# Kernel tuning notes

Measured on AMD Instinct MI355X. Metric: run time of the kernel, lower is better.

## Reference

```python
import jax, jax.numpy as jnp
import numpy as np

STRIDE = 2
PAD = 1
K = 4
OUT_PAD = 0


def setup_inputs() -> dict:
    key = jax.random.key(0)
    k1, k2, k3, k4 = jax.random.split(key, 4)
    x = jax.random.normal(k1, (16, 64, 128, 128), dtype=jnp.float32)
    # torch ConvTranspose2d weight layout: [in_channels, out_channels, kH, kW]
    w = jax.random.normal(k2, (64, 32, 4, 4), dtype=jnp.float32) * 0.05
    conv_b = jax.random.normal(k3, (32,), dtype=jnp.float32) * 0.05
    bias = jax.random.normal(k4, (1, 1, 1, 1), dtype=jnp.float32)
    return {"x": x, "w": w, "conv_b": conv_b, "bias": bias}


def conv_transpose2d(x, w, conv_b):
    # Equivalent of torch ConvTranspose2d(k=4, s=2, p=1, op=0):
    # dilate input by stride, pad by k-1-p (+op on trailing side), conv with flipped kernel.
    lo = K - 1 - PAD
    hi = K - 1 - PAD + OUT_PAD
    w_oihw = jnp.flip(w, axis=(2, 3)).transpose(1, 0, 2, 3)  # [Cout, Cin, kH, kW]
    y = jax.lax.conv_general_dilated(
        x, w_oihw,
        window_strides=(1, 1),
        padding=((lo, hi), (lo, hi)),
        lhs_dilation=(STRIDE, STRIDE),
        dimension_numbers=("NCHW", "OIHW", "NCHW"),
    )
    return y + conv_b[None, :, None, None]


def reference(x, w, conv_b, bias):
    y = conv_transpose2d(x, w, conv_b)          # [N, Cout, H', W']
    y = jnp.min(y, axis=1, keepdims=True)       # channel-min -> [N,1,H',W']
    y = jnp.sum(y, axis=2, keepdims=True)       # height-sum  -> [N,1,1,W']
    # kernel uses tanh-based GELU approximation
    return jax.nn.gelu(y, approximate=True) + bias
```

## Files before the change

kernel.cpp:

```cpp
#include <hip/hip_runtime.h>
#include <math.h>

typedef __attribute__((ext_vector_type(8))) short short8;
typedef __attribute__((ext_vector_type(16))) float f32x16;

#define XS_STRIDE 72

__device__ __forceinline__ short f2bf(float f) {
    union { float f; unsigned u; } v; v.f = f;
    unsigned r = (v.u + 0x7FFFu + ((v.u >> 16) & 1u)) >> 16;
    return (short)r;
}

__global__ void zero_acc(float* __restrict__ acc) {
    acc[blockIdx.x * 256 + threadIdx.x] = 0.f;
}

__global__ void build_wfrag(const float* __restrict__ w, short* __restrict__ wfrag) {
    int idx = blockIdx.x * 256 + threadIdx.x;
    int j    = idx & 7;
    int lane = (idx >> 3) & 63;
    int q    = (idx >> 9) & 15;
    int p    = idx >> 13;
    int co = lane & 31, half = lane >> 5;
    int ci = (q & 3) * 16 + half * 8 + j;
    int t = q >> 2, a = t >> 1, b = t & 1;
    int ph = p >> 1, pw = p & 1;
    int kh = 2 * a + 1 - ph, kw = 2 * b + 1 - pw;
    wfrag[idx] = f2bf(w[((ci * 32 + co) * 4 + kh) * 4 + kw]);
}

__global__ __launch_bounds__(256, 4) void convt_mfma(
    const float* __restrict__ x, const short* __restrict__ wfrag,
    const float* __restrict__ conv_b, float* __restrict__ acc4096)
{
    __shared__ short xs[4][66][XS_STRIDE];
    __shared__ float minbuf[2][4][64];

    int blk = blockIdx.x;
    int jh = blk & 1;
    int i0 = ((blk >> 1) & 63) * 2;
    int n  = blk >> 7;
    int t  = threadIdx.x;

    {
        int col  = t & 63;
        int cih  = (t >> 6) * 4;
        int gcol = jh * 64 + col;
        for (int r = 0; r < 4; ++r) {
            int gi = i0 - 1 + r;
            bool rowok = (unsigned)gi < 128u;
            int gic = rowok ? gi : 0;
            for (int g = 0; g < 4; ++g) {
                int ci = g * 16 + cih;
                const float* px = x + (((size_t)(n * 64 + ci) * 128 + gic) * 128 + gcol);
                float v0 = rowok ? px[0]     : 0.f;
                float v1 = rowok ? px[16384] : 0.f;
                float v2 = rowok ? px[32768] : 0.f;
                float v3 = rowok ? px[49152] : 0.f;
                union { short s[4]; unsigned long long u; } pk;
                pk.s[0] = f2bf(v0); pk.s[1] = f2bf(v1);
                pk.s[2] = f2bf(v2); pk.s[3] = f2bf(v3);
                *(unsigned long long*)&xs[r][col + 1][ci] = pk.u;
            }
        }
        {
            int r = t >> 6, ci = t & 63, gi = i0 - 1 + r;
            for (int side = 0; side < 2; ++side) {
                int gc = jh * 64 + (side ? 64 : -1);
                float v = ((unsigned)gi < 128u && (unsigned)gc < 128u)
                        ? x[((size_t)(n * 64 + ci) * 128 + gi) * 128 + gc] : 0.f;
                xs[r][side ? 65 : 0][ci] = f2bf(v);
            }
        }
    }
    __syncthreads();

    int wv = t >> 6, lane = t & 63;
    int ph = wv >> 1, pw = wv & 1;
    int ln = lane & 31, half = lane >> 5;

    short8 af[16];
    const short8* wf = (const short8*)(wfrag + wv * 8192);
    #pragma unroll
    for (int q = 0; q < 16; ++q) af[q] = wf[q * 64 + lane];

    float cb[16];
    #pragma unroll
    for (int reg = 0; reg < 16; ++reg) {
        int co = (reg & 3) + 8 * (reg >> 2) + 4 * half;
        cb[reg] = conv_b[co];
    }

    #pragma unroll
    for (int rp = 0; rp < 2; ++rp) {
        for (int j0 = 0; j0 < 64; j0 += 32) {
            f32x16 acc;
            #pragma unroll
            for (int reg = 0; reg < 16; ++reg) acc[reg] = cb[reg];
            #pragma unroll
            for (int q = 0; q < 16; ++q) {
                int tq = q >> 2, a = tq >> 1, b = tq & 1;
                int ridx = rp + 1 + ph - a;
                int colp = j0 + ln + (pw - b) + 1;
                int ci0  = (q & 3) * 16 + half * 8;
                const short8* bp = (const short8*)&xs[ridx][colp][ci0];
                acc = __builtin_amdgcn_mfma_f32_32x32x16_bf16(af[q], *bp, acc, 0, 0, 0);
            }
            float mn = acc[0];
            #pragma unroll
            for (int reg = 1; reg < 16; ++reg) mn = fminf(mn, acc[reg]);
            mn = fminf(mn, __shfl_xor(mn, 32, 64));
            if (half == 0) minbuf[rp][wv][j0 + ln] = mn;
        }
    }
    __syncthreads();

    {
        int rp  = t >> 7;
        int pw2 = (t >> 6) & 1;
        int jl  = t & 63;
        float v = minbuf[rp][pw2][jl] + minbuf[rp][2 + pw2][jl];
        int ow = ((jh * 64 + jl) << 1) | pw2;
        atomicAdd(&acc4096[n * 256 + ow], v);
    }
}

__global__ void finalize(const float* __restrict__ acc4096,
                         const float* __restrict__ bias, float* __restrict__ out)
{
    int idx = blockIdx.x * 256 + threadIdx.x;
    float s = acc4096[idx];
    float u = 0.7978845608028654f * (s + 0.044715f * s * s * s);
    out[idx] = 0.5f * s * (1.f + tanhf(u)) + bias[0];
}

extern "C" void kernel_launch(void* const* d_in, const int* in_sizes, int n_in,
                              void* d_out, int out_size, void* d_ws, size_t ws_size,
                              hipStream_t stream) {
    const float* x      = (const float*)d_in[0];
    const float* w      = (const float*)d_in[1];
    const float* conv_b = (const float*)d_in[2];
    const float* bias   = (const float*)d_in[3];
    float* out = (float*)d_out;

    float* acc   = (float*)d_ws;
    short* wfrag = (short*)((char*)d_ws + 16384);

    hipLaunchKernelGGL(zero_acc, dim3(16), dim3(256), 0, stream, acc);
    hipLaunchKernelGGL(build_wfrag, dim3(128), dim3(256), 0, stream, w, wfrag);
    hipLaunchKernelGGL(convt_mfma, dim3(16 * 64 * 2), dim3(256), 0, stream,
                       x, wfrag, conv_b, acc);
    hipLaunchKernelGGL(finalize, dim3(16), dim3(256), 0, stream,
                       acc, bias, out);
}
```

Measured before the change: 135.5 us.

## Fuse prep kernels and fold finalize into last-block epilogue

Merges the zero and weight-fragment kernels into a single prep launch and removes the separate finalize launch. The last conv block to finish, detected with a global atomic counter, applies GELU and bias to the accumulated sums. Each block also pre-sums both row pairs before its atomicAdd, halving the atomics. This cuts two launches and the gaps between them, at the cost of a threadfence and counter atomic per block plus a serial epilogue run by one block.

```diff
diff --git a/kernel.cpp b/kernel.cpp
--- a/kernel.cpp
+++ b/kernel.cpp
@@ -5,6 +5,7 @@
 typedef __attribute__((ext_vector_type(16))) float f32x16;
 
 #define XS_STRIDE 72
+#define NBLOCKS (16 * 64 * 2)
 
 __device__ __forceinline__ short f2bf(float f) {
     union { float f; unsigned u; } v; v.f = f;
@@ -12,30 +13,36 @@
     return (short)r;
 }
 
-__global__ void zero_acc(float* __restrict__ acc) {
-    acc[blockIdx.x * 256 + threadIdx.x] = 0.f;
-}
-
-__global__ void build_wfrag(const float* __restrict__ w, short* __restrict__ wfrag) {
-    int idx = blockIdx.x * 256 + threadIdx.x;
-    int j    = idx & 7;
-    int lane = (idx >> 3) & 63;
-    int q    = (idx >> 9) & 15;
-    int p    = idx >> 13;
-    int co = lane & 31, half = lane >> 5;
-    int ci = (q & 3) * 16 + half * 8 + j;
-    int t = q >> 2, a = t >> 1, b = t & 1;
-    int ph = p >> 1, pw = p & 1;
-    int kh = 2 * a + 1 - ph, kw = 2 * b + 1 - pw;
-    wfrag[idx] = f2bf(w[((ci * 32 + co) * 4 + kh) * 4 + kw]);
+__global__ void prep(const float* __restrict__ w, short* __restrict__ wfrag,
+                     float* __restrict__ acc, unsigned* __restrict__ counter) {
+    int b = blockIdx.x, t = threadIdx.x;
+    if (b < 128) {
+        int idx = b * 256 + t;
+        int j    = idx & 7;
+        int lane = (idx >> 3) & 63;
+        int q    = (idx >> 9) & 15;
+        int p    = idx >> 13;
+        int co = lane & 31, half = lane >> 5;
+        int ci = (q & 3) * 16 + half * 8 + j;
+        int tp = q >> 2, a = tp >> 1, bb = tp & 1;
+        int ph = p >> 1, pw = p & 1;
+        int kh = 2 * a + 1 - ph, kw = 2 * bb + 1 - pw;
+        wfrag[idx] = f2bf(w[((ci * 32 + co) * 4 + kh) * 4 + kw]);
+    } else {
+        acc[(b - 128) * 256 + t] = 0.f;
+        if (b == 128 && t == 0) *counter = 0u;
+    }
 }
 
 __global__ __launch_bounds__(256, 4) void convt_mfma(
     const float* __restrict__ x, const short* __restrict__ wfrag,
-    const float* __restrict__ conv_b, float* __restrict__ acc4096)
+    const float* __restrict__ conv_b, const float* __restrict__ bias,
+    float* __restrict__ acc4096, unsigned* __restrict__ counter,
+    float* __restrict__ out)
 {
     __shared__ short xs[4][66][XS_STRIDE];
     __shared__ float minbuf[2][4][64];
+    __shared__ unsigned lastflag;
 
     int blk = blockIdx.x;
     int jh = blk & 1;
@@ -116,23 +123,32 @@
     }
     __syncthreads();
 
-    {
-        int rp  = t >> 7;
+    if (t < 128) {
         int pw2 = (t >> 6) & 1;
         int jl  = t & 63;
-        float v = minbuf[rp][pw2][jl] + minbuf[rp][2 + pw2][jl];
+        float v = minbuf[0][pw2][jl] + minbuf[0][2 + pw2][jl]
+                + minbuf[1][pw2][jl] + minbuf[1][2 + pw2][jl];
         int ow = ((jh * 64 + jl) << 1) | pw2;
         atomicAdd(&acc4096[n * 256 + ow], v);
     }
-}
+    __threadfence();
+    __syncthreads();
 
-__global__ void finalize(const float* __restrict__ acc4096,
-                         const float* __restrict__ bias, float* __restrict__ out)
-{
-    int idx = blockIdx.x * 256 + threadIdx.x;
-    float s = acc4096[idx];
-    float u = 0.7978845608028654f * (s + 0.044715f * s * s * s);
-    out[idx] = 0.5f * s * (1.f + tanhf(u)) + bias[0];
+    if (t == 0) {
+        unsigned old = __hip_atomic_fetch_add(counter, 1u, __ATOMIC_ACQ_REL,
+                                              __HIP_MEMORY_SCOPE_AGENT);
+        lastflag = (old == (unsigned)(NBLOCKS - 1)) ? 1u : 0u;
+    }
+    __syncthreads();
+    if (lastflag) {
+        float b0 = bias[0];
+        for (int k = t; k < 4096; k += 256) {
+            float s = __hip_atomic_load(&acc4096[k], __ATOMIC_RELAXED,
+                                        __HIP_MEMORY_SCOPE_AGENT);
+            float u = 0.7978845608028654f * (s + 0.044715f * s * s * s);
+            out[k] = 0.5f * s * (1.f + tanhf(u)) + b0;
+        }
+    }
 }
 
 extern "C" void kernel_launch(void* const* d_in, const int* in_sizes, int n_in,
@@ -144,13 +160,11 @@
     const float* bias   = (const float*)d_in[3];
     float* out = (float*)d_out;
 
-    float* acc   = (float*)d_ws;
-    short* wfrag = (short*)((char*)d_ws + 16384);
+    float*    acc     = (float*)d_ws;
+    unsigned* counter = (unsigned*)((char*)d_ws + 16384);
+    short*    wfrag   = (short*)((char*)d_ws + 16448);
 
-    hipLaunchKernelGGL(zero_acc, dim3(16), dim3(256), 0, stream, acc);
-    hipLaunchKernelGGL(build_wfrag, dim3(128), dim3(256), 0, stream, w, wfrag);
-    hipLaunchKernelGGL(convt_mfma, dim3(16 * 64 * 2), dim3(256), 0, stream,
-                       x, wfrag, conv_b, acc);
-    hipLaunchKernelGGL(finalize, dim3(16), dim3(256), 0, stream,
-                       acc, bias, out);
+    hipLaunchKernelGGL(prep, dim3(144), dim3(256), 0, stream, w, wfrag, acc, counter);
+    hipLaunchKernelGGL(convt_mfma, dim3(NBLOCKS), dim3(256), 0, stream,
+                       x, wfrag, conv_b, bias, acc, counter, out);
 }
```

Result: slower. 298.8 us (+120.6%).

## Fuse all stages into one persistent cooperative kernel with grid sync

Applied to the files above, without the earlier changes.

Replaces the four launches (zero, weight-fragment build, conv, finalize) with one persistent cooperative kernel. Each block builds its bf16 weight fragments directly from w, loops over work items, and writes deterministic per-row-pair partials instead of atomics. After a grid-wide sync, 16 blocks reduce the partials and apply GELU plus bias. This removes launch overhead and atomic contention, at the cost of redundant weight conversion per block, a grid-sync barrier and a synchronous occupancy query on the host.

```diff
diff --git a/kernel.cpp b/kernel.cpp
--- a/kernel.cpp
+++ b/kernel.cpp
@@ -1,10 +1,14 @@
 #include <hip/hip_runtime.h>
+#include <hip/hip_cooperative_groups.h>
 #include <math.h>
+
+namespace cg = cooperative_groups;
 
 typedef __attribute__((ext_vector_type(8))) short short8;
 typedef __attribute__((ext_vector_type(16))) float f32x16;
 
 #define XS_STRIDE 72
+#define NITEMS (16 * 64 * 2)
 
 __device__ __forceinline__ short f2bf(float f) {
     union { float f; unsigned u; } v; v.f = f;
@@ -12,127 +16,121 @@
     return (short)r;
 }
 
-__global__ void zero_acc(float* __restrict__ acc) {
-    acc[blockIdx.x * 256 + threadIdx.x] = 0.f;
-}
-
-__global__ void build_wfrag(const float* __restrict__ w, short* __restrict__ wfrag) {
-    int idx = blockIdx.x * 256 + threadIdx.x;
-    int j    = idx & 7;
-    int lane = (idx >> 3) & 63;
-    int q    = (idx >> 9) & 15;
-    int p    = idx >> 13;
-    int co = lane & 31, half = lane >> 5;
-    int ci = (q & 3) * 16 + half * 8 + j;
-    int t = q >> 2, a = t >> 1, b = t & 1;
-    int ph = p >> 1, pw = p & 1;
-    int kh = 2 * a + 1 - ph, kw = 2 * b + 1 - pw;
-    wfrag[idx] = f2bf(w[((ci * 32 + co) * 4 + kh) * 4 + kw]);
-}
-
-__global__ __launch_bounds__(256, 4) void convt_mfma(
-    const float* __restrict__ x, const short* __restrict__ wfrag,
-    const float* __restrict__ conv_b, float* __restrict__ acc4096)
+__global__ __launch_bounds__(256, 4) void convt_fused(
+    const float* __restrict__ x, const float* __restrict__ w,
+    const float* __restrict__ conv_b, const float* __restrict__ bias,
+    float* __restrict__ partial, float* __restrict__ out)
 {
     __shared__ short xs[4][66][XS_STRIDE];
     __shared__ float minbuf[2][4][64];
 
-    int blk = blockIdx.x;
-    int jh = blk & 1;
-    int i0 = ((blk >> 1) & 63) * 2;
-    int n  = blk >> 7;
-    int t  = threadIdx.x;
-
-    {
-        int col  = t & 63;
-        int cih  = (t >> 6) * 4;
-        int gcol = jh * 64 + col;
-        for (int r = 0; r < 4; ++r) {
-            int gi = i0 - 1 + r;
-            bool rowok = (unsigned)gi < 128u;
-            int gic = rowok ? gi : 0;
-            for (int g = 0; g < 4; ++g) {
-                int ci = g * 16 + cih;
-                const float* px = x + (((size_t)(n * 64 + ci) * 128 + gic) * 128 + gcol);
-                float v0 = rowok ? px[0]     : 0.f;
-                float v1 = rowok ? px[16384] : 0.f;
-                float v2 = rowok ? px[32768] : 0.f;
-                float v3 = rowok ? px[49152] : 0.f;
-                union { short s[4]; unsigned long long u; } pk;
-                pk.s[0] = f2bf(v0); pk.s[1] = f2bf(v1);
-                pk.s[2] = f2bf(v2); pk.s[3] = f2bf(v3);
-                *(unsigned long long*)&xs[r][col + 1][ci] = pk.u;
-            }
-        }
-        {
-            int r = t >> 6, ci = t & 63, gi = i0 - 1 + r;
-            for (int side = 0; side < 2; ++side) {
-                int gc = jh * 64 + (side ? 64 : -1);
-                float v = ((unsigned)gi < 128u && (unsigned)gc < 128u)
-                        ? x[((size_t)(n * 64 + ci) * 128 + gi) * 128 + gc] : 0.f;
-                xs[r][side ? 65 : 0][ci] = f2bf(v);
-            }
-        }
-    }
-    __syncthreads();
-
+    int t = threadIdx.x;
     int wv = t >> 6, lane = t & 63;
     int ph = wv >> 1, pw = wv & 1;
     int ln = lane & 31, half = lane >> 5;
 
     short8 af[16];
-    const short8* wf = (const short8*)(wfrag + wv * 8192);
     #pragma unroll
-    for (int q = 0; q < 16; ++q) af[q] = wf[q * 64 + lane];
-
+    for (int q = 0; q < 16; ++q) {
+        int tq = q >> 2, a = tq >> 1, b = tq & 1;
+        int kh = 2 * a + 1 - ph, kw = 2 * b + 1 - pw;
+        int cib = (q & 3) * 16 + half * 8;
+        #pragma unroll
+        for (int j = 0; j < 8; ++j)
+            af[q][j] = f2bf(w[(((cib + j) * 32 + ln) * 4 + kh) * 4 + kw]);
+    }
     float cb[16];
     #pragma unroll
-    for (int reg = 0; reg < 16; ++reg) {
-        int co = (reg & 3) + 8 * (reg >> 2) + 4 * half;
-        cb[reg] = conv_b[co];
+    for (int reg = 0; reg < 16; ++reg)
+        cb[reg] = conv_b[(reg & 3) + 8 * (reg >> 2) + 4 * half];
+
+    for (int item = blockIdx.x; item < NITEMS; item += gridDim.x) {
+        int jh = item & 1;
+        int i0 = ((item >> 1) & 63) * 2;
+        int n  = item >> 7;
+
+        {
+            int col  = t & 63;
+            int cih  = (t >> 6) * 4;
+            int gcol = jh * 64 + col;
+            for (int r = 0; r < 4; ++r) {
+                int gi = i0 - 1 + r;
+                bool rowok = (unsigned)gi < 128u;
+                int gic = rowok ? gi : 0;
+                #pragma unroll
+                for (int g = 0; g < 4; ++g) {
+                    int ci = g * 16 + cih;
+                    const float* px = x + (((size_t)(n * 64 + ci) * 128 + gic) * 128 + gcol);
+                    float v0 = rowok ? px[0]     : 0.f;
+                    float v1 = rowok ? px[16384] : 0.f;
+                    float v2 = rowok ? px[32768] : 0.f;
+                    float v3 = rowok ? px[49152] : 0.f;
+                    union { short s[4]; unsigned long long u; } pk;
+                    pk.s[0] = f2bf(v0); pk.s[1] = f2bf(v1);
+                    pk.s[2] = f2bf(v2); pk.s[3] = f2bf(v3);
+                    *(unsigned long long*)&xs[r][col + 1][ci] = pk.u;
+                }
+            }
+            {
+                int r = t >> 6, ci = t & 63, gi = i0 - 1 + r;
+                for (int side = 0; side < 2; ++side) {
+                    int gc = jh * 64 + (side ? 64 : -1);
+                    float v = ((unsigned)gi < 128u && (unsigned)gc < 128u)
+                            ? x[((size_t)(n * 64 + ci) * 128 + gi) * 128 + gc] : 0.f;
+                    xs[r][side ? 65 : 0][ci] = f2bf(v);
+                }
+            }
+        }
+        __syncthreads();
+
+        #pragma unroll
+        for (int rp = 0; rp < 2; ++rp) {
+            for (int j0 = 0; j0 < 64; j0 += 32) {
+                f32x16 acc;
+                #pragma unroll
+                for (int reg = 0; reg < 16; ++reg) acc[reg] = cb[reg];
+                #pragma unroll
+                for (int q = 0; q < 16; ++q) {
+                    int tq = q >> 2, a = tq >> 1, b = tq & 1;
+                    int ridx = rp + 1 + ph - a;
+                    int colp = j0 + ln + (pw - b) + 1;
+                    int ci0  = (q & 3) * 16 + half * 8;
+                    const short8* bp = (const short8*)&xs[ridx][colp][ci0];
+                    acc = __builtin_amdgcn_mfma_f32_32x32x16_bf16(af[q], *bp, acc, 0, 0, 0);
+                }
+                float mn = acc[0];
+                #pragma unroll
+                for (int reg = 1; reg < 16; ++reg) mn = fminf(mn, acc[reg]);
+                mn = fminf(mn, __shfl_xor(mn, 32, 64));
+                if (half == 0) minbuf[rp][wv][j0 + ln] = mn;
+            }
+        }
+        __syncthreads();
+
+        if (t < 128) {
+            int pw2 = (t >> 6) & 1;
+            int jl  = t & 63;
+            float v = minbuf[0][pw2][jl] + minbuf[0][2 + pw2][jl]
+                    + minbuf[1][pw2][jl] + minbuf[1][2 + pw2][jl];
+            int ow = ((jh * 64 + jl) << 1) | pw2;
+            partial[((size_t)(n * 256) + ow) * 64 + (i0 >> 1)] = v;
+        }
     }
 
-    #pragma unroll
-    for (int rp = 0; rp < 2; ++rp) {
-        for (int j0 = 0; j0 < 64; j0 += 32) {
-            f32x16 acc;
-            #pragma unroll
-            for (int reg = 0; reg < 16; ++reg) acc[reg] = cb[reg];
-            #pragma unroll
-            for (int q = 0; q < 16; ++q) {
-                int tq = q >> 2, a = tq >> 1, b = tq & 1;
-                int ridx = rp + 1 + ph - a;
-                int colp = j0 + ln + (pw - b) + 1;
-                int ci0  = (q & 3) * 16 + half * 8;
-                const short8* bp = (const short8*)&xs[ridx][colp][ci0];
-                acc = __builtin_amdgcn_mfma_f32_32x32x16_bf16(af[q], *bp, acc, 0, 0, 0);
-            }
-            float mn = acc[0];
-            #pragma unroll
-            for (int reg = 1; reg < 16; ++reg) mn = fminf(mn, acc[reg]);
-            mn = fminf(mn, __shfl_xor(mn, 32, 64));
-            if (half == 0) minbuf[rp][wv][j0 + ln] = mn;
+    cg::this_grid().sync();
+
+    if (blockIdx.x < 16) {
+        int k = blockIdx.x * 256 + t;
+        const float4* p = (const float4*)(partial + (size_t)k * 64);
+        float s = 0.f;
+        #pragma unroll
+        for (int q = 0; q < 16; ++q) {
+            float4 v = p[q];
+            s += v.x + v.y + v.z + v.w;
         }
+        float u = 0.7978845608028654f * (s + 0.044715f * s * s * s);
+        out[k] = 0.5f * s * (1.f + tanhf(u)) + bias[0];
     }
-    __syncthreads();
-
-    {
-        int rp  = t >> 7;
-        int pw2 = (t >> 6) & 1;
-        int jl  = t & 63;
-        float v = minbuf[rp][pw2][jl] + minbuf[rp][2 + pw2][jl];
-        int ow = ((jh * 64 + jl) << 1) | pw2;
-        atomicAdd(&acc4096[n * 256 + ow], v);
-    }
-}
-
-__global__ void finalize(const float* __restrict__ acc4096,
-                         const float* __restrict__ bias, float* __restrict__ out)
-{
-    int idx = blockIdx.x * 256 + threadIdx.x;
-    float s = acc4096[idx];
-    float u = 0.7978845608028654f * (s + 0.044715f * s * s * s);
-    out[idx] = 0.5f * s * (1.f + tanhf(u)) + bias[0];
 }
 
 extern "C" void kernel_launch(void* const* d_in, const int* in_sizes, int n_in,
@@ -142,15 +140,17 @@
     const float* w      = (const float*)d_in[1];
     const float* conv_b = (const float*)d_in[2];
     const float* bias   = (const float*)d_in[3];
-    float* out = (float*)d_out;
+    float* out     = (float*)d_out;
+    float* partial = (float*)d_ws;
 
-    float* acc   = (float*)d_ws;
-    short* wfrag = (short*)((char*)d_ws + 16384);
+    int maxb = 4;
+    hipOccupancyMaxActiveBlocksPerMultiprocessor(&maxb, (const void*)convt_fused, 256, 0);
+    if (maxb < 1) maxb = 1;
+    int nb = maxb * 256;
+    if (nb > NITEMS) nb = NITEMS;
 
-    hipLaunchKernelGGL(zero_acc, dim3(16), dim3(256), 0, stream, acc);
-    hipLaunchKernelGGL(build_wfrag, dim3(128), dim3(256), 0, stream, w, wfrag);
-    hipLaunchKernelGGL(convt_mfma, dim3(16 * 64 * 2), dim3(256), 0, stream,
-                       x, wfrag, conv_b, acc);
-    hipLaunchKernelGGL(finalize, dim3(16), dim3(256), 0, stream,
-                       acc, bias, out);
+    void* args[] = {(void*)&x, (void*)&w, (void*)&conv_b, (void*)&bias,
+                    (void*)&partial, (void*)&out};
+    hipLaunchCooperativeKernel((void*)convt_fused, dim3(nb), dim3(256),
+                               args, 0, stream);
 }
```

Measured after the change: 259.5 us. +91.5%, slower.

## Pre-transpose input to NHWC bf16 and read MFMA operands directly from global

Applied to the files above, without the earlier changes.

Adds a prep kernel that converts x from NCHW fp32 into an NHWC bf16 buffer in workspace. The same kernel also builds the weight fragments and zeroes the accumulator, merging three launches into one. The conv kernel drops its LDS staging and the transposing loads, and instead reads 16-byte channel vectors for each MFMA straight from global memory with bounds masking. The cost is an extra full write and re-read of the transposed input (about 33 MB) and uncoalesced-by-block global loads inside the MFMA loop, which rely on cache reuse. The final min reduction is also folded so each output column issues one atomic instead of two.

```diff
diff --git a/kernel.cpp b/kernel.cpp
--- a/kernel.cpp
+++ b/kernel.cpp
@@ -4,7 +4,7 @@
 typedef __attribute__((ext_vector_type(8))) short short8;
 typedef __attribute__((ext_vector_type(16))) float f32x16;
 
-#define XS_STRIDE 72
+#define NITEMS (16 * 64 * 2)
 
 __device__ __forceinline__ short f2bf(float f) {
     union { float f; unsigned u; } v; v.f = f;
@@ -12,29 +12,49 @@
     return (short)r;
 }
 
-__global__ void zero_acc(float* __restrict__ acc) {
-    acc[blockIdx.x * 256 + threadIdx.x] = 0.f;
+__global__ __launch_bounds__(256) void prep_transpose(
+    const float* __restrict__ x, short* __restrict__ xT,
+    const float* __restrict__ w, short* __restrict__ wfrag,
+    float* __restrict__ acc)
+{
+    int b = blockIdx.x, t = threadIdx.x;
+    int h = b & 127, n = b >> 7;
+    int wv = t >> 6, l = t & 63;
+
+    for (int m = 0; m < 4; ++m) {
+        int task = m * 4 + wv;
+        int oct = task >> 1, wt = task & 1;
+        int gw = wt * 64 + l;
+        short8 o;
+        #pragma unroll
+        for (int k = 0; k < 8; ++k) {
+            float v = x[(((size_t)(n * 64 + oct * 8 + k)) * 128 + h) * 128 + gw];
+            o[k] = f2bf(v);
+        }
+        *(short8*)(xT + (((size_t)(n * 128 + h) * 128 + gw) * 64 + oct * 8)) = o;
+    }
+
+    if (b < 128) {
+        int idx = b * 256 + t;
+        int j    = idx & 7;
+        int lane = (idx >> 3) & 63;
+        int q    = (idx >> 9) & 15;
+        int p    = idx >> 13;
+        int co = lane & 31, half = lane >> 5;
+        int ci = (q & 3) * 16 + half * 8 + j;
+        int tq = q >> 2, a = tq >> 1, bb = tq & 1;
+        int ph = p >> 1, pw = p & 1;
+        int kh = 2 * a + 1 - ph, kw = 2 * bb + 1 - pw;
+        wfrag[idx] = f2bf(w[((ci * 32 + co) * 4 + kh) * 4 + kw]);
+    } else if (b < 144) {
+        acc[(b - 128) * 256 + t] = 0.f;
+    }
 }
 
-__global__ void build_wfrag(const float* __restrict__ w, short* __restrict__ wfrag) {
-    int idx = blockIdx.x * 256 + threadIdx.x;
-    int j    = idx & 7;
-    int lane = (idx >> 3) & 63;
-    int q    = (idx >> 9) & 15;
-    int p    = idx >> 13;
-    int co = lane & 31, half = lane >> 5;
-    int ci = (q & 3) * 16 + half * 8 + j;
-    int t = q >> 2, a = t >> 1, b = t & 1;
-    int ph = p >> 1, pw = p & 1;
-    int kh = 2 * a + 1 - ph, kw = 2 * b + 1 - pw;
-    wfrag[idx] = f2bf(w[((ci * 32 + co) * 4 + kh) * 4 + kw]);
-}
-
-__global__ __launch_bounds__(256, 4) void convt_mfma(
-    const float* __restrict__ x, const short* __restrict__ wfrag,
+__global__ __launch_bounds__(256, 4) void convt_direct(
+    const short* __restrict__ xT, const short* __restrict__ wfrag,
     const float* __restrict__ conv_b, float* __restrict__ acc4096)
 {
-    __shared__ short xs[4][66][XS_STRIDE];
     __shared__ float minbuf[2][4][64];
 
     int blk = blockIdx.x;
@@ -42,40 +62,6 @@
     int i0 = ((blk >> 1) & 63) * 2;
     int n  = blk >> 7;
     int t  = threadIdx.x;
-
-    {
-        int col  = t & 63;
-        int cih  = (t >> 6) * 4;
-        int gcol = jh * 64 + col;
-        for (int r = 0; r < 4; ++r) {
-            int gi = i0 - 1 + r;
-            bool rowok = (unsigned)gi < 128u;
-            int gic = rowok ? gi : 0;
-            for (int g = 0; g < 4; ++g) {
-                int ci = g * 16 + cih;
-                const float* px = x + (((size_t)(n * 64 + ci) * 128 + gic) * 128 + gcol);
-                float v0 = rowok ? px[0]     : 0.f;
-                float v1 = rowok ? px[16384] : 0.f;
-                float v2 = rowok ? px[32768] : 0.f;
-                float v3 = rowok ? px[49152] : 0.f;
-                union { short s[4]; unsigned long long u; } pk;
-                pk.s[0] = f2bf(v0); pk.s[1] = f2bf(v1);
-                pk.s[2] = f2bf(v2); pk.s[3] = f2bf(v3);
-                *(unsigned long long*)&xs[r][col + 1][ci] = pk.u;
-            }
-        }
-        {
-            int r = t >> 6, ci = t & 63, gi = i0 - 1 + r;
-            for (int side = 0; side < 2; ++side) {
-                int gc = jh * 64 + (side ? 64 : -1);
-                float v = ((unsigned)gi < 128u && (unsigned)gc < 128u)
-                        ? x[((size_t)(n * 64 + ci) * 128 + gi) * 128 + gc] : 0.f;
-                xs[r][side ? 65 : 0][ci] = f2bf(v);
-            }
-        }
-    }
-    __syncthreads();
-
     int wv = t >> 6, lane = t & 63;
     int ph = wv >> 1, pw = wv & 1;
     int ln = lane & 31, half = lane >> 5;
@@ -87,26 +73,47 @@
 
     float cb[16];
     #pragma unroll
-    for (int reg = 0; reg < 16; ++reg) {
-        int co = (reg & 3) + 8 * (reg >> 2) + 4 * half;
-        cb[reg] = conv_b[co];
-    }
+    for (int reg = 0; reg < 16; ++reg)
+        cb[reg] = conv_b[(reg & 3) + 8 * (reg >> 2) + 4 * half];
+
+    const short8 ZERO8 = {0, 0, 0, 0, 0, 0, 0, 0};
+    const short* xn = xT + (size_t)n * 128 * 128 * 64;
 
     #pragma unroll
     for (int rp = 0; rp < 2; ++rp) {
+        int gi0 = i0 + rp + ph;
+        int gi1 = gi0 - 1;
+        bool rok0 = (unsigned)gi0 < 128u;
+        bool rok1 = (unsigned)gi1 < 128u;
+        const short* row0 = xn + (size_t)min(max(gi0, 0), 127) * (128 * 64);
+        const short* row1 = xn + (size_t)min(max(gi1, 0), 127) * (128 * 64);
+
         for (int j0 = 0; j0 < 64; j0 += 32) {
+            int gwq0 = jh * 64 + j0 + ln + pw;
+            int gwq1 = gwq0 - 1;
+            bool cok0 = (unsigned)gwq0 < 128u;
+            bool cok1 = (unsigned)gwq1 < 128u;
+            int gw0 = min(max(gwq0, 0), 127);
+            int gw1 = min(max(gwq1, 0), 127);
+
             f32x16 acc;
             #pragma unroll
             for (int reg = 0; reg < 16; ++reg) acc[reg] = cb[reg];
+
             #pragma unroll
             for (int q = 0; q < 16; ++q) {
-                int tq = q >> 2, a = tq >> 1, b = tq & 1;
-                int ridx = rp + 1 + ph - a;
-                int colp = j0 + ln + (pw - b) + 1;
-                int ci0  = (q & 3) * 16 + half * 8;
-                const short8* bp = (const short8*)&xs[ridx][colp][ci0];
-                acc = __builtin_amdgcn_mfma_f32_32x32x16_bf16(af[q], *bp, acc, 0, 0, 0);
+                int tq = q >> 2;
+                const short* rbase = (tq & 2) ? row1 : row0;
+                bool rok          = (tq & 2) ? rok1 : rok0;
+                int gw            = (tq & 1) ? gw1 : gw0;
+                bool cok          = (tq & 1) ? cok1 : cok0;
+                int ci0 = (q & 3) * 16 + half * 8;
+                const short8* bp = (const short8*)(rbase + ((size_t)gw * 64 + ci0));
+                short8 bv = *bp;
+                if (!(rok && cok)) bv = ZERO8;
+                acc = __builtin_amdgcn_mfma_f32_32x32x16_bf16(af[q], bv, acc, 0, 0, 0);
             }
+
             float mn = acc[0];
             #pragma unroll
             for (int reg = 1; reg < 16; ++reg) mn = fminf(mn, acc[reg]);
@@ -116,11 +123,11 @@
     }
     __syncthreads();
 
-    {
-        int rp  = t >> 7;
+    if (t < 128) {
         int pw2 = (t >> 6) & 1;
         int jl  = t & 63;
-        float v = minbuf[rp][pw2][jl] + minbuf[rp][2 + pw2][jl];
+        float v = minbuf[0][pw2][jl] + minbuf[0][2 + pw2][jl]
+                + minbuf[1][pw2][jl] + minbuf[1][2 + pw2][jl];
         int ow = ((jh * 64 + jl) << 1) | pw2;
         atomicAdd(&acc4096[n * 256 + ow], v);
     }
@@ -146,11 +153,12 @@
 
     float* acc   = (float*)d_ws;
     short* wfrag = (short*)((char*)d_ws + 16384);
+    short* xT    = (short*)((char*)d_ws + 131072);
 
-    hipLaunchKernelGGL(zero_acc, dim3(16), dim3(256), 0, stream, acc);
-    hipLaunchKernelGGL(build_wfrag, dim3(128), dim3(256), 0, stream, w, wfrag);
-    hipLaunchKernelGGL(convt_mfma, dim3(16 * 64 * 2), dim3(256), 0, stream,
-                       x, wfrag, conv_b, acc);
+    hipLaunchKernelGGL(prep_transpose, dim3(16 * 128), dim3(256), 0, stream,
+                       x, xT, w, wfrag, acc);
+    hipLaunchKernelGGL(convt_direct, dim3(NITEMS), dim3(256), 0, stream,
+                       xT, wfrag, conv_b, acc);
     hipLaunchKernelGGL(finalize, dim3(16), dim3(256), 0, stream,
                        acc, bias, out);
 }
```

Result: slower. 176.5 us (+30.3%).
